# Optimization experiments

Measured on AMD Instinct MI355X. Metric: run time of the kernel, lower is better.

## Reference

```python
import jax, jax.numpy as jnp
import numpy as np

N = 50000   # nodes
E = 800000  # edges
D = 128     # feature / hidden dim
G = 64      # graphs in batch
L = 3       # GCN layers
EPS = 1e-5  # LayerNorm eps (torch default)


def setup_inputs() -> dict:
    key = jax.random.key(0)
    ks = jax.random.split(key, 6)
    x = jax.random.normal(ks[0], (N, D), dtype=jnp.float32)
    edge_index = jax.random.randint(ks[1], (2, E), 0, N)
    batch = jnp.sort(jax.random.randint(ks[2], (N,), 0, G))
    Ws = jax.random.normal(ks[3], (L, D, D), dtype=jnp.float32) / np.sqrt(D).astype(np.float32)
    bs = jnp.zeros((L, D), dtype=jnp.float32)
    gammas = jnp.ones((L, D), dtype=jnp.float32)
    betas = jnp.zeros((L, D), dtype=jnp.float32)
    return {"x": x, "edge_index": edge_index, "batch": batch,
            "Ws": Ws, "bs": bs, "gammas": gammas, "betas": betas,
            "num_graphs": G}


def _layernorm(h, g, b):
    mu = jnp.mean(h, axis=-1, keepdims=True)
    var = jnp.mean((h - mu) ** 2, axis=-1, keepdims=True)
    return g * (h - mu) * jax.lax.rsqrt(var + EPS) + b


def reference(x, edge_index, batch, Ws, bs, gammas, betas, num_graphs):
    n = x.shape[0]
    loop = jnp.arange(n)
    # GCNConv adds self-loops; symmetric normalization on augmented graph
    src = jnp.concatenate([edge_index[0], loop])
    dst = jnp.concatenate([edge_index[1], loop])
    deg = jax.ops.segment_sum(jnp.ones_like(dst, dtype=x.dtype), dst, num_segments=n)
    dinv = jax.lax.rsqrt(jnp.maximum(deg, 1.0))  # deg >= 1 via self-loops
    norm_e = dinv[src] * dinv[dst]               # [E+N]

    h = x
    for i in range(Ws.shape[0]):
        hw = h @ Ws[i]                           # [N, D] dense GEMM
        msg = hw[src] * norm_e[:, None]          # gather + edge scale
        h = jax.ops.segment_sum(msg, dst, num_segments=n) + bs[i]  # scatter-add
        h = jax.nn.relu(_layernorm(h, gammas[i], betas[i]))
        # dropout is identity in eval mode

    # global mean pool over graph ids
    s = jax.ops.segment_sum(h, batch, num_segments=num_graphs)
    cnt = jax.ops.segment_sum(jnp.ones((n,), x.dtype), batch, num_segments=num_graphs)
    return s / jnp.maximum(cnt, 1.0)[:, None]
```

## Files before the change

kernel.cpp:

```cpp
#include <hip/hip_runtime.h>
#include <math.h>


#define NDIM 128
#define LN_EPS 1e-5f
#define NGRAPH 64
#define EPB 2048

typedef __attribute__((ext_vector_type(8))) short short8;
typedef __attribute__((ext_vector_type(4))) float f32x4;

__device__ __forceinline__ ushort f2bf(float f) {
    unsigned u = __float_as_uint(f);
    return (ushort)((u + 0x7FFF + ((u >> 16) & 1)) >> 16);
}
__device__ __forceinline__ float bf2f(ushort b) {
    return __uint_as_float(((unsigned)b) << 16);
}

__device__ __forceinline__ uint block_excl_scan(uint v, uint* s) {
    int t = threadIdx.x;
    s[t] = v; __syncthreads();
    #pragma unroll
    for (int off = 1; off < 256; off <<= 1) {
        uint x = (t >= off) ? s[t - off] : 0u;
        __syncthreads();
        s[t] += x;
        __syncthreads();
    }
    uint incl = s[t];
    __syncthreads();
    return incl - v;
}


__global__ __launch_bounds__(256) void k_h1(const int* __restrict__ dst, uint* __restrict__ hist, int E) {
    __shared__ uint h[256];
    int t = threadIdx.x, b = blockIdx.x;
    h[t] = 0; __syncthreads();
    int e0 = b * EPB;
    #pragma unroll
    for (int i = 0; i < 8; i++) {
        int e = e0 + i * 256 + t;
        if (e < E) atomicAdd(&h[((uint)dst[e]) >> 8], 1u);
    }
    __syncthreads();
    hist[(size_t)b * 256 + t] = h[t];
}

__global__ __launch_bounds__(256) void k_colscan(uint* __restrict__ hist, uint* __restrict__ colsum, int EB) {
    __shared__ uint s[256];
    int t = threadIdx.x, j = blockIdx.x;
    uint v0 = (2 * t     < EB) ? hist[(size_t)(2 * t) * 256 + j] : 0u;
    uint v1 = (2 * t + 1 < EB) ? hist[(size_t)(2 * t + 1) * 256 + j] : 0u;
    uint pair = v0 + v1;
    uint excl = block_excl_scan(pair, s);
    if (2 * t < EB)     hist[(size_t)(2 * t) * 256 + j] = excl;
    if (2 * t + 1 < EB) hist[(size_t)(2 * t + 1) * 256 + j] = excl + v0;
    if (t == 255) colsum[j] = excl + pair;
}

__global__ __launch_bounds__(256) void k_binscan(const uint* __restrict__ colsum, uint* __restrict__ eoff,
                                                 uint* __restrict__ cbase) {
    __shared__ uint s[256];
    int t = threadIdx.x;
    uint total = colsum[t];
    uint er = block_excl_scan(total, s);
    eoff[t] = er;
    if (t == 255) eoff[256] = er + total;
    uint ep = block_excl_scan((total + 3u) & ~3u, s);
    cbase[t] = ep + 768u * (uint)t;
}

__global__ __launch_bounds__(256) void k_scatter1(const int* __restrict__ src, const int* __restrict__ dst,
                                                  const uint* __restrict__ hist, const uint* __restrict__ eoff,
                                                  uint* __restrict__ ebuf, int E) {
    __shared__ uint off[256];
    __shared__ uint cur[256];
    int t = threadIdx.x, b = blockIdx.x;
    off[t] = eoff[t] + hist[(size_t)b * 256 + t];
    cur[t] = 0;
    __syncthreads();
    int e0 = b * EPB;
    #pragma unroll
    for (int i = 0; i < 8; i++) {
        int e = e0 + i * 256 + t;
        if (e < E) {
            uint d = (uint)dst[e], sv = (uint)src[e];
            uint bin = d >> 8;
            uint r = atomicAdd(&cur[bin], 1u);
            ebuf[off[bin] + r] = (d << 16) | sv;
        }
    }
}

__global__ __launch_bounds__(256) void k_sort2(const uint* __restrict__ ebuf, const uint* __restrict__ eoff,
                                               const uint* __restrict__ cbase, const int* __restrict__ batch,
                                               ushort* __restrict__ csr, int* __restrict__ base,
                                               int* __restrict__ deg, float* __restrict__ dinv,
                                               int* __restrict__ gstart, int* __restrict__ gend, int N) {
    __shared__ uint h[256], nbase[256], s[256];
    int t = threadIdx.x, b = blockIdx.x;
    uint lo = eoff[b];
    int cnt = (int)(eoff[b + 1] - lo);
    h[t] = 0; __syncthreads();
    for (int i = t; i < cnt; i += 256)
        atomicAdd(&h[(ebuf[lo + i] >> 16) & 255u], 1u);
    __syncthreads();
    uint dg = h[t];
    uint excl = block_excl_scan((dg + 3u) & ~3u, s);
    uint myb = cbase[b] + excl;
    nbase[t] = myb;
    int n = b * 256 + t;
    if (n < N) {
        base[n] = (int)myb;
        deg[n] = (int)dg;
        dinv[n] = rsqrtf((float)(dg + 1u));
        int g = batch[n];
        if (n == 0 || batch[n - 1] != g) gstart[g] = n;
        if (n == N - 1 || batch[n + 1] != g) gend[g] = n + 1;
    }
    h[t] = 0;
    __syncthreads();
    for (int i = t; i < cnt; i += 256) {
        uint e = ebuf[lo + i];
        uint bin = (e >> 16) & 255u;
        uint r = atomicAdd(&h[bin], 1u);
        csr[nbase[bin] + r] = (ushort)(e & 0xFFFFu);
    }
}


__global__ __launch_bounds__(256) void k_wt(const float* __restrict__ W, ushort* __restrict__ Wt) {
    int l = blockIdx.x;
    const float* w = W + (size_t)l * NDIM * NDIM;
    char* o = (char*)(Wt + (size_t)l * NDIM * NDIM);
    for (int idx = threadIdx.x; idx < NDIM * NDIM; idx += 256) {
        int k = idx >> 7, n = idx & 127;
        int byte = ((n * NDIM + k) * 2) ^ ((n & 7) << 4);
        *(ushort*)(o + byte) = f2bf(w[idx]);
    }
}


template <bool AF32>
__global__ __launch_bounds__(256) void k_gemm(const void* __restrict__ Ap, const ushort* __restrict__ Wt,
                                              ushort* __restrict__ C, const float* __restrict__ dinv, int N) {
    __shared__ char sW[32768];
    __shared__ ushort sC[64 * NDIM];
    int tid = threadIdx.x;
    {
        const float4* g = (const float4*)Wt;
        float4* s = (float4*)sW;
        #pragma unroll
        for (int i = 0; i < 8; i++) s[tid + 256 * i] = g[tid + 256 * i];
    }
    __syncthreads();

    int wave = tid >> 6, lane = tid & 63;
    int l15 = lane & 15, lhi = lane >> 4;
    int rw = blockIdx.x * 64 + wave * 16;

    f32x4 acc[8];
    #pragma unroll
    for (int n = 0; n < 8; n++) acc[n] = f32x4{0.f, 0.f, 0.f, 0.f};

    const float*  Af = (const float*)Ap;
    const ushort* Ab = (const ushort*)Ap;

    #pragma unroll
    for (int ks = 0; ks < 4; ks++) {
        int k = ks * 32 + lhi * 8;
        short8 a = short8{};
        int r = rw + l15;
        if (r < N) {
            if (AF32) {
                float4 v0 = *(const float4*)&Af[(size_t)r * NDIM + k];
                float4 v1 = *(const float4*)&Af[(size_t)r * NDIM + k + 4];
                short8 t;
                t[0] = (short)f2bf(v0.x); t[1] = (short)f2bf(v0.y);
                t[2] = (short)f2bf(v0.z); t[3] = (short)f2bf(v0.w);
                t[4] = (short)f2bf(v1.x); t[5] = (short)f2bf(v1.y);
                t[6] = (short)f2bf(v1.z); t[7] = (short)f2bf(v1.w);
                a = t;
            } else {
                a = *(const short8*)&Ab[(size_t)r * NDIM + k];
            }
        }
        #pragma unroll
        for (int n = 0; n < 8; n++) {
            int nn = n * 16 + l15;
            int byte = (nn * 256 + k * 2) ^ ((nn & 7) << 4);
            short8 b = *(const short8*)(sW + byte);
            acc[n] = __builtin_amdgcn_mfma_f32_16x16x32_bf16(a, b, acc[n], 0, 0, 0);
        }
    }

    #pragma unroll
    for (int r = 0; r < 4; r++) {
        int row = rw + lhi * 4 + r;
        float dn = (row < N) ? dinv[row] : 0.f;
        #pragma unroll
        for (int n = 0; n < 8; n++)
            sC[(wave * 16 + lhi * 4 + r) * NDIM + n * 16 + l15] = f2bf(acc[n][r] * dn);
    }
    __syncthreads();
    int row0 = blockIdx.x * 64;
    #pragma unroll
    for (int i = 0; i < 4; i++) {
        int flat = tid + i * 256;
        int row = flat >> 4, c8 = (flat & 15) * 8;
        int gr = row0 + row;
        if (gr < N)
            *(short8*)&C[(size_t)gr * NDIM + c8] = *(const short8*)&sC[row * NDIM + c8];
    }
}


__global__ __launch_bounds__(256) void k_agg(const ushort* __restrict__ hw, ushort* __restrict__ out,
                                             const float* __restrict__ dinv, const int* __restrict__ base,
                                             const int* __restrict__ deg, const ushort* __restrict__ csr,
                                             const float* __restrict__ bias, const float* __restrict__ gamma,
                                             const float* __restrict__ beta, int N) {
    int gtid = blockIdx.x * 256 + threadIdx.x;
    int n = gtid >> 5;
    int l4 = threadIdx.x & 31;
    if (n >= N) return;

    const ushort4* hv = (const ushort4*)hw;
    ushort4 sv = hv[(size_t)n * 32 + l4];
    float a0 = bf2f(sv.x), a1 = bf2f(sv.y), a2 = bf2f(sv.z), a3 = bf2f(sv.w);

    int b0 = base[n], dg = deg[n];
    int nfull = dg & ~7;
    ushort4 sa, sb;
    if (nfull > 0) {
        sa = *(const ushort4*)&csr[b0];
        sb = *(const ushort4*)&csr[b0 + 4];
    }
    for (int i = 0; i < nfull; i += 8) {
        ushort4 ca = sa, cb = sb;
        if (i + 8 < nfull) {
            sa = *(const ushort4*)&csr[b0 + i + 8];
            sb = *(const ushort4*)&csr[b0 + i + 12];
        }
        ushort4 t0 = hv[(size_t)ca.x * 32 + l4];
        ushort4 t1 = hv[(size_t)ca.y * 32 + l4];
        ushort4 t2 = hv[(size_t)ca.z * 32 + l4];
        ushort4 t3 = hv[(size_t)ca.w * 32 + l4];
        ushort4 t4 = hv[(size_t)cb.x * 32 + l4];
        ushort4 t5 = hv[(size_t)cb.y * 32 + l4];
        ushort4 t6 = hv[(size_t)cb.z * 32 + l4];
        ushort4 t7 = hv[(size_t)cb.w * 32 + l4];
        a0 += bf2f(t0.x) + bf2f(t1.x) + bf2f(t2.x) + bf2f(t3.x)
            + bf2f(t4.x) + bf2f(t5.x) + bf2f(t6.x) + bf2f(t7.x);
        a1 += bf2f(t0.y) + bf2f(t1.y) + bf2f(t2.y) + bf2f(t3.y)
            + bf2f(t4.y) + bf2f(t5.y) + bf2f(t6.y) + bf2f(t7.y);
        a2 += bf2f(t0.z) + bf2f(t1.z) + bf2f(t2.z) + bf2f(t3.z)
            + bf2f(t4.z) + bf2f(t5.z) + bf2f(t6.z) + bf2f(t7.z);
        a3 += bf2f(t0.w) + bf2f(t1.w) + bf2f(t2.w) + bf2f(t3.w)
            + bf2f(t4.w) + bf2f(t5.w) + bf2f(t6.w) + bf2f(t7.w);
    }
    for (int i = nfull; i < dg; i++) {
        int s = csr[b0 + i];
        ushort4 t = hv[(size_t)s * 32 + l4];
        a0 += bf2f(t.x); a1 += bf2f(t.y); a2 += bf2f(t.z); a3 += bf2f(t.w);
    }

    float dn = dinv[n];
    a0 *= dn; a1 *= dn; a2 *= dn; a3 *= dn;

    float4 bv = ((const float4*)bias)[l4];
    a0 += bv.x; a1 += bv.y; a2 += bv.z; a3 += bv.w;

    float s1 = a0 + a1 + a2 + a3;
    float s2 = a0 * a0 + a1 * a1 + a2 * a2 + a3 * a3;
    #pragma unroll
    for (int o = 1; o < 32; o <<= 1) {
        s1 += __shfl_xor(s1, o);
        s2 += __shfl_xor(s2, o);
    }
    float mu = s1 * (1.f / NDIM);
    float var = s2 * (1.f / NDIM) - mu * mu;
    float rs = rsqrtf(var + LN_EPS);

    float4 gv = ((const float4*)gamma)[l4];
    float4 be = ((const float4*)beta)[l4];
    ushort4 y;
    y.x = f2bf(fmaxf(gv.x * (a0 - mu) * rs + be.x, 0.f));
    y.y = f2bf(fmaxf(gv.y * (a1 - mu) * rs + be.y, 0.f));
    y.z = f2bf(fmaxf(gv.z * (a2 - mu) * rs + be.z, 0.f));
    y.w = f2bf(fmaxf(gv.w * (a3 - mu) * rs + be.w, 0.f));
    ((ushort4*)out)[(size_t)n * 32 + l4] = y;
}


__global__ __launch_bounds__(128) void k_pool(const ushort* __restrict__ h, const int* __restrict__ batch,
                                              float* __restrict__ out, int N) {
    int d = threadIdx.x;
    int start = blockIdx.x * 64;
    if (start >= N) return;
    int end = min(start + 64, N);
    int cur = batch[start];
    float sum = 0.f;
    for (int n = start; n < end; n++) {
        int g = batch[n];
        if (g != cur) {
            atomicAdd(&out[cur * NDIM + d], sum);
            sum = 0.f;
            cur = g;
        }
        sum += bf2f(h[(size_t)n * NDIM + d]);
    }
    atomicAdd(&out[cur * NDIM + d], sum);
}

__global__ __launch_bounds__(256) void k_div(float* __restrict__ out, const int* __restrict__ gstart,
                                             const int* __restrict__ gend) {
    int i = blockIdx.x * 256 + threadIdx.x;
    if (i < NGRAPH * NDIM) {
        int g = i >> 7;
        float c = (float)(gend[g] - gstart[g]);
        out[i] /= fmaxf(c, 1.f);
    }
}


extern "C" void kernel_launch(void* const* d_in, const int* in_sizes, int n_in,
                              void* d_out, int out_size, void* d_ws, size_t ws_size,
                              hipStream_t stream) {
    const float* x      = (const float*)d_in[0];
    const int*   ei     = (const int*)d_in[1];
    const int*   batch  = (const int*)d_in[2];
    const float* Ws     = (const float*)d_in[3];
    const float* bs     = (const float*)d_in[4];
    const float* gammas = (const float*)d_in[5];
    const float* betas  = (const float*)d_in[6];
    float* out = (float*)d_out;

    int N = in_sizes[0] / NDIM;
    int E = in_sizes[1] / 2;
    const int* src = ei;
    const int* dst = ei + E;
    int EB = (E + EPB - 1) / EPB;
    int NB = (N + 255) / 256;

    char* w = (char*)d_ws;
    auto alloc = [&](size_t bytes) { char* p = w; w += (bytes + 255) & ~(size_t)255; return p; };
    int*    deg    = (int*)alloc((size_t)N * 4);
    int*    base   = (int*)alloc((size_t)N * 4);
    float*  dinv   = (float*)alloc((size_t)N * 4);
    uint*   hist   = (uint*)alloc((size_t)EB * 256 * 4);
    uint*   colsum = (uint*)alloc(256 * 4);
    uint*   eoff   = (uint*)alloc(257 * 4);
    uint*   cbase  = (uint*)alloc(256 * 4);
    uint*   ebuf   = (uint*)alloc((size_t)E * 4);
    ushort* csr    = (ushort*)alloc(((size_t)E + 256u * 772u) * 2);
    int*    gse    = (int*)alloc(2 * NGRAPH * 4);
    int*    gstart = gse;
    int*    gend   = gse + NGRAPH;
    ushort* Wt     = (ushort*)alloc((size_t)3 * NDIM * NDIM * 2);
    ushort* bufA   = (ushort*)alloc((size_t)N * NDIM * 2);
    ushort* bufB   = (ushort*)alloc((size_t)N * NDIM * 2);

    hipMemsetAsync(out, 0, (size_t)NGRAPH * NDIM * 4, stream);

    k_h1<<<EB, 256, 0, stream>>>(dst, hist, E);
    k_colscan<<<256, 256, 0, stream>>>(hist, colsum, EB);
    k_binscan<<<1, 256, 0, stream>>>(colsum, eoff, cbase);
    k_scatter1<<<EB, 256, 0, stream>>>(src, dst, hist, eoff, ebuf, E);
    k_sort2<<<NB, 256, 0, stream>>>(ebuf, eoff, cbase, batch, csr, base, deg, dinv, gstart, gend, N);
    k_wt<<<3, 256, 0, stream>>>(Ws, Wt);

    int gGemm = (N + 63) / 64;
    int gAgg  = (N * 32 + 255) / 256;
    for (int l = 0; l < 3; l++) {
        const ushort* wl = Wt + (size_t)l * NDIM * NDIM;
        if (l == 0)
            k_gemm<true><<<gGemm, 256, 0, stream>>>((const void*)x, wl, bufB, dinv, N);
        else
            k_gemm<false><<<gGemm, 256, 0, stream>>>((const void*)bufA, wl, bufB, dinv, N);
        k_agg<<<gAgg, 256, 0, stream>>>(bufB, bufA, dinv, base, deg, csr,
                                        bs + l * NDIM, gammas + l * NDIM, betas + l * NDIM, N);
    }

    k_pool<<<(N + 63) / 64, 128, 0, stream>>>(bufA, batch, out, N);
    k_div<<<(NGRAPH * NDIM + 255) / 256, 256, 0, stream>>>(out, gstart, gend);
}
```

Before: 290.2 us.

## Fold scans and weight conversion into neighbouring kernels and rewrite pooling per graph

The single-block bin scan moves into k_scatter1 and k_sort2, where each block recomputes it redundantly. The weight transpose and bf16 conversion run as three extra blocks of k_sort2. The atomic pool, its divide kernel and the output memset are replaced by one pooling kernel with one block per graph, using vectorized loads and a shared-memory reduction. This cuts four launches and the atomic traffic, at the cost of redundant scan work in every block and only 64 blocks for pooling.

```diff
diff --git a/kernel.cpp b/kernel.cpp
--- a/kernel.cpp
+++ b/kernel.cpp
@@ -8,6 +8,7 @@
 #define EPB 2048
 
 typedef __attribute__((ext_vector_type(8))) short short8;
+typedef __attribute__((ext_vector_type(8))) ushort ushort8;
 typedef __attribute__((ext_vector_type(4))) float f32x4;
 
 __device__ __forceinline__ ushort f2bf(float f) {
@@ -60,25 +61,15 @@
     if (t == 255) colsum[j] = excl + pair;
 }
 
-__global__ __launch_bounds__(256) void k_binscan(const uint* __restrict__ colsum, uint* __restrict__ eoff,
-                                                 uint* __restrict__ cbase) {
+__global__ __launch_bounds__(256) void k_scatter1(const int* __restrict__ src, const int* __restrict__ dst,
+                                                  const uint* __restrict__ hist, const uint* __restrict__ colsum,
+                                                  uint* __restrict__ ebuf, int E) {
     __shared__ uint s[256];
-    int t = threadIdx.x;
-    uint total = colsum[t];
-    uint er = block_excl_scan(total, s);
-    eoff[t] = er;
-    if (t == 255) eoff[256] = er + total;
-    uint ep = block_excl_scan((total + 3u) & ~3u, s);
-    cbase[t] = ep + 768u * (uint)t;
-}
-
-__global__ __launch_bounds__(256) void k_scatter1(const int* __restrict__ src, const int* __restrict__ dst,
-                                                  const uint* __restrict__ hist, const uint* __restrict__ eoff,
-                                                  uint* __restrict__ ebuf, int E) {
     __shared__ uint off[256];
     __shared__ uint cur[256];
     int t = threadIdx.x, b = blockIdx.x;
-    off[t] = eoff[t] + hist[(size_t)b * 256 + t];
+    uint er = block_excl_scan(colsum[t], s);
+    off[t] = er + hist[(size_t)b * 256 + t];
     cur[t] = 0;
     __syncthreads();
     int e0 = b * EPB;
@@ -94,23 +85,43 @@
     }
 }
 
-__global__ __launch_bounds__(256) void k_sort2(const uint* __restrict__ ebuf, const uint* __restrict__ eoff,
-                                               const uint* __restrict__ cbase, const int* __restrict__ batch,
+__global__ __launch_bounds__(256) void k_sort2(const uint* __restrict__ ebuf, const uint* __restrict__ colsum,
+                                               const int* __restrict__ batch,
                                                ushort* __restrict__ csr, int* __restrict__ base,
                                                int* __restrict__ deg, float* __restrict__ dinv,
-                                               int* __restrict__ gstart, int* __restrict__ gend, int N) {
-    __shared__ uint h[256], nbase[256], s[256];
+                                               int* __restrict__ gstart, int* __restrict__ gend,
+                                               const float* __restrict__ Ws, ushort* __restrict__ Wt,
+                                               int N, int NB) {
+    __shared__ uint h[256], nb[256], s[256], er_arr[256], ep_arr[256];
     int t = threadIdx.x, b = blockIdx.x;
-    uint lo = eoff[b];
-    int cnt = (int)(eoff[b + 1] - lo);
+    if (b >= NB) {
+        int l = b - NB;
+        const float* wsrc = Ws + (size_t)l * NDIM * NDIM;
+        char* o = (char*)(Wt + (size_t)l * NDIM * NDIM);
+        for (int idx = t; idx < NDIM * NDIM; idx += 256) {
+            int k = idx >> 7, nn = idx & 127;
+            int byte = ((nn * NDIM + k) * 2) ^ ((nn & 7) << 4);
+            *(ushort*)(o + byte) = f2bf(wsrc[idx]);
+        }
+        return;
+    }
+    uint total = colsum[t];
+    uint er = block_excl_scan(total, s);
+    er_arr[t] = er;
+    uint ep = block_excl_scan((total + 3u) & ~3u, s);
+    ep_arr[t] = ep;
+    __syncthreads();
+    uint lo = er_arr[b];
+    int cnt = (int)colsum[b];
+    uint cb = ep_arr[b] + 768u * (uint)b;
     h[t] = 0; __syncthreads();
     for (int i = t; i < cnt; i += 256)
         atomicAdd(&h[(ebuf[lo + i] >> 16) & 255u], 1u);
     __syncthreads();
     uint dg = h[t];
     uint excl = block_excl_scan((dg + 3u) & ~3u, s);
-    uint myb = cbase[b] + excl;
-    nbase[t] = myb;
+    uint myb = cb + excl;
+    nb[t] = myb;
     int n = b * 256 + t;
     if (n < N) {
         base[n] = (int)myb;
@@ -120,25 +131,12 @@
         if (n == 0 || batch[n - 1] != g) gstart[g] = n;
         if (n == N - 1 || batch[n + 1] != g) gend[g] = n + 1;
     }
-    h[t] = 0;
-    __syncthreads();
+    h[t] = 0; __syncthreads();
     for (int i = t; i < cnt; i += 256) {
         uint e = ebuf[lo + i];
         uint bin = (e >> 16) & 255u;
         uint r = atomicAdd(&h[bin], 1u);
-        csr[nbase[bin] + r] = (ushort)(e & 0xFFFFu);
-    }
-}
-
-
-__global__ __launch_bounds__(256) void k_wt(const float* __restrict__ W, ushort* __restrict__ Wt) {
-    int l = blockIdx.x;
-    const float* w = W + (size_t)l * NDIM * NDIM;
-    char* o = (char*)(Wt + (size_t)l * NDIM * NDIM);
-    for (int idx = threadIdx.x; idx < NDIM * NDIM; idx += 256) {
-        int k = idx >> 7, n = idx & 127;
-        int byte = ((n * NDIM + k) * 2) ^ ((n & 7) << 4);
-        *(ushort*)(o + byte) = f2bf(w[idx]);
+        csr[nb[bin] + r] = (ushort)(e & 0xFFFFu);
     }
 }
 
@@ -295,33 +293,27 @@
 }
 
 
-__global__ __launch_bounds__(128) void k_pool(const ushort* __restrict__ h, const int* __restrict__ batch,
-                                              float* __restrict__ out, int N) {
-    int d = threadIdx.x;
-    int start = blockIdx.x * 64;
-    if (start >= N) return;
-    int end = min(start + 64, N);
-    int cur = batch[start];
-    float sum = 0.f;
-    for (int n = start; n < end; n++) {
-        int g = batch[n];
-        if (g != cur) {
-            atomicAdd(&out[cur * NDIM + d], sum);
-            sum = 0.f;
-            cur = g;
-        }
-        sum += bf2f(h[(size_t)n * NDIM + d]);
-    }
-    atomicAdd(&out[cur * NDIM + d], sum);
-}
-
-__global__ __launch_bounds__(256) void k_div(float* __restrict__ out, const int* __restrict__ gstart,
-                                             const int* __restrict__ gend) {
-    int i = blockIdx.x * 256 + threadIdx.x;
-    if (i < NGRAPH * NDIM) {
-        int g = i >> 7;
-        float c = (float)(gend[g] - gstart[g]);
-        out[i] /= fmaxf(c, 1.f);
+__global__ __launch_bounds__(256) void k_pool2(const ushort* __restrict__ h, const int* __restrict__ gstart,
+                                               const int* __restrict__ gend, float* __restrict__ out) {
+    __shared__ float ps[16][128];
+    int t = threadIdx.x, g = blockIdx.x;
+    int st = gstart[g], en = gend[g];
+    int rslot = t >> 4, dc = (t & 15) * 8;
+    float acc[8] = {0.f, 0.f, 0.f, 0.f, 0.f, 0.f, 0.f, 0.f};
+    for (int r = st + rslot; r < en; r += 16) {
+        ushort8 v = *(const ushort8*)&h[(size_t)r * NDIM + dc];
+        #pragma unroll
+        for (int j = 0; j < 8; j++) acc[j] += bf2f(v[j]);
+    }
+    #pragma unroll
+    for (int j = 0; j < 8; j++) ps[rslot][dc + j] = acc[j];
+    __syncthreads();
+    if (t < 128) {
+        float s = 0.f;
+        #pragma unroll
+        for (int k = 0; k < 16; k++) s += ps[k][t];
+        float c = (float)(en - st);
+        out[g * NDIM + t] = s / fmaxf(c, 1.f);
     }
 }
 
@@ -352,8 +344,6 @@
     float*  dinv   = (float*)alloc((size_t)N * 4);
     uint*   hist   = (uint*)alloc((size_t)EB * 256 * 4);
     uint*   colsum = (uint*)alloc(256 * 4);
-    uint*   eoff   = (uint*)alloc(257 * 4);
-    uint*   cbase  = (uint*)alloc(256 * 4);
     uint*   ebuf   = (uint*)alloc((size_t)E * 4);
     ushort* csr    = (ushort*)alloc(((size_t)E + 256u * 772u) * 2);
     int*    gse    = (int*)alloc(2 * NGRAPH * 4);
@@ -363,14 +353,11 @@
     ushort* bufA   = (ushort*)alloc((size_t)N * NDIM * 2);
     ushort* bufB   = (ushort*)alloc((size_t)N * NDIM * 2);
 
-    hipMemsetAsync(out, 0, (size_t)NGRAPH * NDIM * 4, stream);
-
     k_h1<<<EB, 256, 0, stream>>>(dst, hist, E);
     k_colscan<<<256, 256, 0, stream>>>(hist, colsum, EB);
-    k_binscan<<<1, 256, 0, stream>>>(colsum, eoff, cbase);
-    k_scatter1<<<EB, 256, 0, stream>>>(src, dst, hist, eoff, ebuf, E);
-    k_sort2<<<NB, 256, 0, stream>>>(ebuf, eoff, cbase, batch, csr, base, deg, dinv, gstart, gend, N);
-    k_wt<<<3, 256, 0, stream>>>(Ws, Wt);
+    k_scatter1<<<EB, 256, 0, stream>>>(src, dst, hist, colsum, ebuf, E);
+    k_sort2<<<NB + 3, 256, 0, stream>>>(ebuf, colsum, batch, csr, base, deg, dinv,
+                                        gstart, gend, Ws, Wt, N, NB);
 
     int gGemm = (N + 63) / 64;
     int gAgg  = (N * 32 + 255) / 256;
@@ -384,6 +371,5 @@
                                         bs + l * NDIM, gammas + l * NDIM, betas + l * NDIM, N);
     }
 
-    k_pool<<<(N + 63) / 64, 128, 0, stream>>>(bufA, batch, out, N);
-    k_div<<<(NGRAPH * NDIM + 255) / 256, 256, 0, stream>>>(out, gstart, gend);
-}
+    k_pool2<<<NGRAPH, 256, 0, stream>>>(bufA, gstart, gend, out);
+}
```

New measurement: 271.1 us. -6.6%, faster.
